# Performance work log

Measured on AMD Instinct MI355X. Metric: run time of the kernel, lower is better.

The kernel has to match this reference:

```python
import jax, jax.numpy as jnp
import numpy as np

SPATIAL_SHAPES = [(80, 80), (40, 40), (20, 20)]  # (h, w) per level; sum(h*w) = 8400


def setup_inputs() -> dict:
    key = jax.random.key(0)
    k1, k2, k3 = jax.random.split(key, 3)
    bs, Lv, nH, c = 16, 8400, 8, 32
    Lq, L, P = 300, 3, 4
    value = jax.random.normal(k1, (bs, Lv, nH, c), dtype=jnp.float32)
    value_spatial_shapes = jnp.asarray(SPATIAL_SHAPES, dtype=jnp.int64)
    sampling_locations = jax.random.uniform(k2, (bs, Lq, nH, L, P, 2), dtype=jnp.float32)
    aw = jax.random.uniform(k3, (bs, Lq, nH, L, P), dtype=jnp.float32)
    attention_weights = aw / jnp.sum(aw, axis=(-2, -1), keepdims=True)
    return {
        "value": value,
        "value_spatial_shapes": value_spatial_shapes,
        "sampling_locations": sampling_locations,
        "attention_weights": attention_weights,
    }


def _sample_level(v, g, h, w):
    """Bilinear zero-padded sampling (grid_sample, align_corners=False).
    v: [bs, h*w, nH, c] (row-major h,w); g: [bs, Lq, nH, P, 2] in [0,1].
    Returns [bs, Lq, P, nH, c]."""
    bs, _, nH, c = v.shape
    Lq, P = g.shape[1], g.shape[3]
    # grid_sample align_corners=False: pixel = ((2*loc-1 + 1)*size - 1)/2 = loc*size - 0.5
    x = g[..., 0] * w - 0.5  # [bs, Lq, nH, P]
    y = g[..., 1] * h - 0.5
    x0 = jnp.floor(x)
    y0 = jnp.floor(y)
    acc = jnp.zeros((bs, Lq, P, nH, c), dtype=v.dtype)
    for dx in (0, 1):
        for dy in (0, 1):
            xi = x0 + dx
            yi = y0 + dy
            wgt = (1.0 - jnp.abs(x - xi)) * (1.0 - jnp.abs(y - yi))
            valid = (xi >= 0) & (xi < w) & (yi >= 0) & (yi < h)
            wgt = jnp.where(valid, wgt, 0.0)  # zero padding
            xc = jnp.clip(xi, 0, w - 1).astype(jnp.int32)
            yc = jnp.clip(yi, 0, h - 1).astype(jnp.int32)
            idx = yc * w + xc  # [bs, Lq, nH, P]
            idx = jnp.transpose(idx, (0, 1, 3, 2)).reshape(bs, Lq * P, nH, 1)
            gathered = jnp.take_along_axis(v, idx, axis=1)  # [bs, Lq*P, nH, c]
            gathered = gathered.reshape(bs, Lq, P, nH, c)
            wgt_t = jnp.transpose(wgt, (0, 1, 3, 2))  # [bs, Lq, P, nH]
            acc = acc + gathered * wgt_t[..., None]
    return acc


def reference(value, value_spatial_shapes, sampling_locations, attention_weights):
    # value_spatial_shapes is static metadata (used for shapes) -> host ints
    shapes = [(int(h), int(w)) for h, w in np.asarray(value_spatial_shapes)]
    bs, _, nH, c = value.shape
    Lq = sampling_locations.shape[1]
    splits = np.cumsum([h * w for h, w in shapes])[:-1]
    value_list = jnp.split(value, splits, axis=1)
    sampled = []
    for lvl, (h, w) in enumerate(shapes):
        g = sampling_locations[:, :, :, lvl]  # [bs, Lq, nH, P, 2]
        sampled.append(_sample_level(value_list[lvl], g, h, w))
    stacked = jnp.stack(sampled, axis=2)  # [bs, Lq, L, P, nH, c]
    out = jnp.einsum('bqlpnc,bqnlp->bqnc', stacked, attention_weights)
    return out.reshape(bs, Lq, nH * c)
```

## Files before the change

### kernel.cpp

```cpp
#include <hip/hip_runtime.h>

#define BS   16
#define LQ   300
#define NH   8
#define C    32
#define LV   8400
#define POS_BYTES 1024

__device__ __forceinline__ void sample_point(
    const char* __restrict__ vbase, float gx, float gy, float aw,
    int W, int H, int off, float4& acc)
{
    const float x = gx * (float)W - 0.5f;
    const float y = gy * (float)H - 0.5f;
    const float xf = floorf(x), yf = floorf(y);
    const int x0 = (int)xf, y0 = (int)yf;
    const int x1 = x0 + 1,  y1 = y0 + 1;
    const float lx = x - xf, ly = y - yf;
    const float hx = 1.f - lx, hy = 1.f - ly;

    float w00 = hx * hy * aw;
    float w10 = lx * hy * aw;
    float w01 = hx * ly * aw;
    float w11 = lx * ly * aw;

    const bool vx0 = (unsigned)x0 < (unsigned)W;
    const bool vx1 = (unsigned)x1 < (unsigned)W;
    const bool vy0 = (unsigned)y0 < (unsigned)H;
    const bool vy1 = (unsigned)y1 < (unsigned)H;
    w00 = (vx0 && vy0) ? w00 : 0.f;
    w10 = (vx1 && vy0) ? w10 : 0.f;
    w01 = (vx0 && vy1) ? w01 : 0.f;
    w11 = (vx1 && vy1) ? w11 : 0.f;

    const int xc0 = min(max(x0, 0), W - 1);
    const int xc1 = min(max(x1, 0), W - 1);
    const int yc0 = min(max(y0, 0), H - 1);
    const int yc1 = min(max(y1, 0), H - 1);

    const int r0 = off + yc0 * W;
    const int r1 = off + yc1 * W;
    const float4 v00 = *(const float4*)(vbase + ((r0 + xc0) << 10));
    const float4 v10 = *(const float4*)(vbase + ((r0 + xc1) << 10));
    const float4 v01 = *(const float4*)(vbase + ((r1 + xc0) << 10));
    const float4 v11 = *(const float4*)(vbase + ((r1 + xc1) << 10));

    acc.x += v00.x * w00 + v10.x * w10 + v01.x * w01 + v11.x * w11;
    acc.y += v00.y * w00 + v10.y * w10 + v01.y * w01 + v11.y * w11;
    acc.z += v00.z * w00 + v10.z * w10 + v01.z * w01 + v11.z * w11;
    acc.w += v00.w * w00 + v10.w * w10 + v01.w * w01 + v11.w * w11;
}

__global__ __launch_bounds__(256, 4) void msda_fwd(
    const float* __restrict__ value,
    const float* __restrict__ loc,
    const float* __restrict__ attw,
    float* __restrict__ out)
{
    __shared__ float4 lds[256];

    const int t  = threadIdx.x;
    const int bq = blockIdx.x;
    const int c4 = t & 7;
    const int h  = (t >> 3) & (NH - 1);
    const int pg = t >> 6;
    const int b  = bq / LQ;

    const float2* lp = (const float2*)(loc + (size_t)(bq * NH + h) * 24);
    const float*  ap = attw + (size_t)(bq * NH + h) * 12;
    const char* vbase = (const char*)value
                      + (size_t)b * LV * POS_BYTES + h * (C * 4) + c4 * 16;

    float4 acc = make_float4(0.f, 0.f, 0.f, 0.f);

#define SAMPLE(i, W_, H_, OFF_) do {                         \
        const float2 g = lp[i];                              \
        sample_point(vbase, g.x, g.y, ap[i], W_, H_, OFF_, acc); \
    } while (0)

    switch (pg) {
    case 0: SAMPLE(0, 80, 80, 0);    SAMPLE(1, 80, 80, 0);    SAMPLE(2,  80, 80, 0);    break;
    case 1: SAMPLE(3, 80, 80, 0);    SAMPLE(4, 40, 40, 6400); SAMPLE(5,  40, 40, 6400); break;
    case 2: SAMPLE(6, 40, 40, 6400); SAMPLE(7, 40, 40, 6400); SAMPLE(8,  20, 20, 8000); break;
    default:SAMPLE(9, 20, 20, 8000); SAMPLE(10,20, 20, 8000); SAMPLE(11, 20, 20, 8000); break;
    }
#undef SAMPLE

    lds[t] = acc;
    __syncthreads();

    if (t < 64) {
        float4 a0 = lds[t];
        float4 a1 = lds[t + 64];
        float4 a2 = lds[t + 128];
        float4 a3 = lds[t + 192];
        float4 r;
        r.x = (a0.x + a1.x) + (a2.x + a3.x);
        r.y = (a0.y + a1.y) + (a2.y + a3.y);
        r.z = (a0.z + a1.z) + (a2.z + a3.z);
        r.w = (a0.w + a1.w) + (a2.w + a3.w);
        ((float4*)out)[(size_t)bq * 64 + t] = r;
    }
}

extern "C" void kernel_launch(void* const* d_in, const int* in_sizes, int n_in,
                              void* d_out, int out_size, void* d_ws, size_t ws_size,
                              hipStream_t stream) {
    const float* value = (const float*)d_in[0];
    const float* loc   = (const float*)d_in[2];
    const float* attw  = (const float*)d_in[3];
    float* out = (float*)d_out;

    const int grid = BS * LQ;
    msda_fwd<<<grid, 256, 0, stream>>>(value, loc, attw, out);
}
```

Baseline: 193.3 us.

## Assign one query per wavefront and drop the LDS point-group reduction

Result: slower. 197.9 us (+2.4%).

```diff
diff --git a/kernel.cpp b/kernel.cpp
--- a/kernel.cpp
+++ b/kernel.cpp
@@ -57,50 +57,38 @@
     const float* __restrict__ attw,
     float* __restrict__ out)
 {
-    __shared__ float4 lds[256];
+    const int t    = threadIdx.x;
+    const int lane = t & 63;
+    const int bq   = blockIdx.x * 4 + (t >> 6);
+    const int c4   = lane & 7;
+    const int h    = lane >> 3;
+    const int b    = bq / LQ;
 
-    const int t  = threadIdx.x;
-    const int bq = blockIdx.x;
-    const int c4 = t & 7;
-    const int h  = (t >> 3) & (NH - 1);
-    const int pg = t >> 6;
-    const int b  = bq / LQ;
-
-    const float2* lp = (const float2*)(loc + (size_t)(bq * NH + h) * 24);
-    const float*  ap = attw + (size_t)(bq * NH + h) * 12;
+    const float4* lp4 = (const float4*)(loc  + (size_t)(bq * NH + h) * 24);
+    const float4* ap4 = (const float4*)(attw + (size_t)(bq * NH + h) * 12);
     const char* vbase = (const char*)value
                       + (size_t)b * LV * POS_BYTES + h * (C * 4) + c4 * 16;
 
+    const float4 L0 = lp4[0], L1 = lp4[1], L2 = lp4[2];
+    const float4 L3 = lp4[3], L4 = lp4[4], L5 = lp4[5];
+    const float4 A0 = ap4[0], A1 = ap4[1], A2 = ap4[2];
+
     float4 acc = make_float4(0.f, 0.f, 0.f, 0.f);
 
-#define SAMPLE(i, W_, H_, OFF_) do {                         \
-        const float2 g = lp[i];                              \
-        sample_point(vbase, g.x, g.y, ap[i], W_, H_, OFF_, acc); \
-    } while (0)
+    sample_point(vbase, L0.x, L0.y, A0.x, 80, 80, 0, acc);
+    sample_point(vbase, L0.z, L0.w, A0.y, 80, 80, 0, acc);
+    sample_point(vbase, L1.x, L1.y, A0.z, 80, 80, 0, acc);
+    sample_point(vbase, L1.z, L1.w, A0.w, 80, 80, 0, acc);
+    sample_point(vbase, L2.x, L2.y, A1.x, 40, 40, 6400, acc);
+    sample_point(vbase, L2.z, L2.w, A1.y, 40, 40, 6400, acc);
+    sample_point(vbase, L3.x, L3.y, A1.z, 40, 40, 6400, acc);
+    sample_point(vbase, L3.z, L3.w, A1.w, 40, 40, 6400, acc);
+    sample_point(vbase, L4.x, L4.y, A2.x, 20, 20, 8000, acc);
+    sample_point(vbase, L4.z, L4.w, A2.y, 20, 20, 8000, acc);
+    sample_point(vbase, L5.x, L5.y, A2.z, 20, 20, 8000, acc);
+    sample_point(vbase, L5.z, L5.w, A2.w, 20, 20, 8000, acc);
 
-    switch (pg) {
-    case 0: SAMPLE(0, 80, 80, 0);    SAMPLE(1, 80, 80, 0);    SAMPLE(2,  80, 80, 0);    break;
-    case 1: SAMPLE(3, 80, 80, 0);    SAMPLE(4, 40, 40, 6400); SAMPLE(5,  40, 40, 6400); break;
-    case 2: SAMPLE(6, 40, 40, 6400); SAMPLE(7, 40, 40, 6400); SAMPLE(8,  20, 20, 8000); break;
-    default:SAMPLE(9, 20, 20, 8000); SAMPLE(10,20, 20, 8000); SAMPLE(11, 20, 20, 8000); break;
-    }
-#undef SAMPLE
-
-    lds[t] = acc;
-    __syncthreads();
-
-    if (t < 64) {
-        float4 a0 = lds[t];
-        float4 a1 = lds[t + 64];
-        float4 a2 = lds[t + 128];
-        float4 a3 = lds[t + 192];
-        float4 r;
-        r.x = (a0.x + a1.x) + (a2.x + a3.x);
-        r.y = (a0.y + a1.y) + (a2.y + a3.y);
-        r.z = (a0.z + a1.z) + (a2.z + a3.z);
-        r.w = (a0.w + a1.w) + (a2.w + a3.w);
-        ((float4*)out)[(size_t)bq * 64 + t] = r;
-    }
+    ((float4*)out)[(size_t)bq * 64 + lane] = acc;
 }
 
 extern "C" void kernel_launch(void* const* d_in, const int* in_sizes, int n_in,
@@ -111,6 +99,6 @@
     const float* attw  = (const float*)d_in[3];
     float* out = (float*)d_out;
 
-    const int grid = BS * LQ;
+    const int grid = BS * LQ / 4;
     msda_fwd<<<grid, 256, 0, stream>>>(value, loc, attw, out);
 }
```
